# Performance work log

Measured on AMD Instinct MI355X. Metric: run time of the kernel, lower is better.

The kernel has to match this reference:

```python
import jax, jax.numpy as jnp
import numpy as np
import math

D_MODEL = 2048
N_HEADS = 16
HEAD_DIM = D_MODEL // N_HEADS  # 128
SEQ = 2048
BATCH = 1


def make_freqs(seq_len, head_dim, theta=10000.0):
    # standard rotary frequencies: freqs_cis = exp(i * t * inv_freq)
    inv_freq = 1.0 / (theta ** (np.arange(0, head_dim, 2, dtype=np.float32) / head_dim))
    t = np.arange(seq_len, dtype=np.float32)
    ang = np.outer(t, inv_freq)  # [seq, head_dim/2]
    return jnp.asarray(np.cos(ang)), jnp.asarray(np.sin(ang))


def setup_inputs() -> dict:
    key = jax.random.key(0)
    ks = jax.random.split(key, 6)
    x = jax.random.normal(ks[0], (BATCH, SEQ, D_MODEL), dtype=jnp.float32)
    freqs_cos, freqs_sin = make_freqs(SEQ, HEAD_DIM)
    # causal additive mask, broadcastable to [b, h, s, s]
    mask = jnp.where(jnp.tril(jnp.ones((SEQ, SEQ), dtype=bool)), 0.0, -1e9).astype(jnp.float32)[None, None]
    scale = 0.02
    wq = jax.random.normal(ks[1], (D_MODEL, D_MODEL), dtype=jnp.float32) * scale
    wk = jax.random.normal(ks[2], (D_MODEL, D_MODEL), dtype=jnp.float32) * scale
    wv = jax.random.normal(ks[3], (D_MODEL, D_MODEL), dtype=jnp.float32) * scale
    wo = jax.random.normal(ks[4], (D_MODEL, D_MODEL), dtype=jnp.float32) * scale
    return {"x": x, "freqs_cos": freqs_cos, "freqs_sin": freqs_sin, "mask": mask,
            "wq": wq, "wk": wk, "wv": wv, "wo": wo}


def _apply_rotary(q, k, cos, sin):
    # q, k: [b, s, h, hd]; cos/sin: [s, hd/2]
    def rot(t):
        tr = t.reshape(*t.shape[:-1], -1, 2)  # [b, s, h, hd/2, 2]
        re, im = tr[..., 0], tr[..., 1]
        c = cos[None, :, None, :]
        s = sin[None, :, None, :]
        # complex multiply (re + i im) * (c + i s)
        out_re = re * c - im * s
        out_im = re * s + im * c
        return jnp.stack([out_re, out_im], axis=-1).reshape(t.shape)
    return rot(q), rot(k)


def reference(x, freqs_cos, freqs_sin, mask, wq, wk, wv, wo):
    b, s, _ = x.shape
    # QKV projections (nn.Linear with no bias: x @ W^T; W is square so use x @ W
    # with W stored already-transposed -- weights here are random so x @ W is faithful math)
    q = (x @ wq).reshape(b, s, N_HEADS, HEAD_DIM)
    k = (x @ wk).reshape(b, s, N_HEADS, HEAD_DIM)
    v = (x @ wv).reshape(b, s, N_HEADS, HEAD_DIM)
    q, k = _apply_rotary(q, k, freqs_cos, freqs_sin)
    # [b, h, s_q, s_k]
    scores = jnp.einsum("bqhd,bkhd->bhqk", q, k) / math.sqrt(HEAD_DIM)
    scores = scores + mask
    probs = jax.nn.softmax(scores.astype(jnp.float32), axis=-1).astype(q.dtype)
    out = jnp.einsum("bhqk,bkhd->bqhd", probs, v).reshape(b, s, N_HEADS * HEAD_DIM)
    return out @ wo
```

## Files before the change

### kernel.cpp

```cpp
#include <hip/hip_runtime.h>
#include <hip/hip_bf16.h>
#include <math.h>

#define SEQ 2048
#define DM 2048
#define NH 16
#define HD 128
#define QKV_N 6144

typedef __bf16 bf16;
typedef __bf16 bf16x8 __attribute__((ext_vector_type(8)));
typedef __bf16 bf16x4v __attribute__((ext_vector_type(4)));
typedef __bf16 bf16x2v __attribute__((ext_vector_type(2)));
typedef float f32x4 __attribute__((ext_vector_type(4)));

__device__ inline int sw_idx(int row, int quad) {
    return (row * 4 + (quad ^ ((row >> 1) & 3))) * 8;
}

__device__ inline void async16(const void* g, void* l) {
    __builtin_amdgcn_global_load_lds((const __attribute__((address_space(1))) void*)g,
                                     (__attribute__((address_space(3))) void*)l, 16, 0, 0);
}

__global__ void k_convert_x(const float* __restrict__ x, bf16* __restrict__ xb) {
    int i = blockIdx.x * 256 + threadIdx.x;
    float4 v = ((const float4*)x)[i];
    bf16x4v o;
    o.x = (bf16)v.x; o.y = (bf16)v.y; o.z = (bf16)v.z; o.w = (bf16)v.w;
    ((bf16x4v*)xb)[i] = o;
}

__global__ void k_transpose_w4(const float* __restrict__ wq, const float* __restrict__ wk,
                               const float* __restrict__ wv, const float* __restrict__ wo,
                               bf16* __restrict__ wT, bf16* __restrict__ woT) {
    __shared__ float tile[32][33];
    const int z = blockIdx.z;
    const float* src = (z == 0) ? wq : (z == 1) ? wk : (z == 2) ? wv : wo;
    bf16* dst = (z < 3) ? (wT + (size_t)z * DM * DM) : woT;
    int tx = threadIdx.x, ty = threadIdx.y;
    int bx = blockIdx.x * 32, by = blockIdx.y * 32;
    tile[ty][tx] = src[(size_t)(by + ty) * DM + bx + tx];
    __syncthreads();
    dst[(size_t)(bx + ty) * DM + by + tx] = (bf16)tile[tx][ty];
}

__global__ void k_post(bf16* __restrict__ qkv, const float* __restrict__ cosT,
                       const float* __restrict__ sinT, bf16* __restrict__ vT) {
    __shared__ bf16 tile[32][33];
    int tx = threadIdx.x, ty = threadIdx.y;
    if (blockIdx.y < 64) {
        int bx = blockIdx.x * 32, by = blockIdx.y * 32;
        tile[ty][tx] = qkv[(size_t)(by + ty) * QKV_N + 2 * DM + bx + tx];
        __syncthreads();
        vT[(size_t)(bx + ty) * SEQ + by + tx] = tile[tx][ty];
    } else {
        int b = (blockIdx.y - 64) * 64 + blockIdx.x;
        int idx = b * 1024 + ty * 32 + tx;
        int i = idx & 63;
        int h = (idx >> 6) & 15;
        int s = idx >> 10;
        float c = cosT[s * 64 + i], sn = sinT[s * 64 + i];
        size_t base = (size_t)s * QKV_N + h * HD + 2 * i;
        bf16x2v q = *(bf16x2v*)&qkv[base];
        float qr = (float)q.x, qi = (float)q.y;
        bf16x2v qo;
        qo.x = (bf16)(qr * c - qi * sn);
        qo.y = (bf16)(qr * sn + qi * c);
        *(bf16x2v*)&qkv[base] = qo;
        bf16x2v k = *(bf16x2v*)&qkv[base + DM];
        float kr = (float)k.x, ki = (float)k.y;
        bf16x2v ko;
        ko.x = (bf16)(kr * c - ki * sn);
        ko.y = (bf16)(kr * sn + ki * c);
        *(bf16x2v*)&qkv[base + DM] = ko;
    }
}

template <typename OutT, int BN>
__global__ __launch_bounds__(256) void k_gemm_bt(const bf16* __restrict__ A,
                                                 const bf16* __restrict__ Bt,
                                                 OutT* __restrict__ C,
                                                 int M, int N, int K) {
    constexpr int NI = BN / 32;
    __shared__ bf16 As[128 * 32];
    __shared__ bf16 Bs[BN * 32];
    const int t = threadIdx.x;
    const int lane = t & 63;
    const int w = t >> 6;
    const int wr = (w >> 1) * 64, wc = (w & 1) * (BN / 2);
    const int l15 = lane & 15, quad = lane >> 4;
    const size_t bm = (size_t)blockIdx.y * 128, bn = (size_t)blockIdx.x * BN;
    f32x4 acc[4][NI];
#pragma unroll
    for (int i = 0; i < 4; ++i)
#pragma unroll
        for (int j = 0; j < NI; ++j) acc[i][j] = (f32x4){0.f, 0.f, 0.f, 0.f};

    const int row0 = t >> 2, row1 = 64 + (t >> 2);
    const int ch = ((t & 3) ^ ((t >> 3) & 3)) * 8;

    for (int kt = 0; kt < K; kt += 32) {
        async16(&A[(bm + row0) * K + kt + ch], &As[t * 8]);
        async16(&A[(bm + row1) * K + kt + ch], &As[(t + 256) * 8]);
        async16(&Bt[(bn + row0) * K + kt + ch], &Bs[t * 8]);
        if (BN == 128)
            async16(&Bt[(bn + row1) * K + kt + ch], &Bs[(t + 256) * 8]);
        __syncthreads();
        bf16x8 af[4], bfm[NI];
#pragma unroll
        for (int mi = 0; mi < 4; ++mi)
            af[mi] = *(const bf16x8*)&As[sw_idx(wr + mi * 16 + l15, quad)];
#pragma unroll
        for (int ni = 0; ni < NI; ++ni)
            bfm[ni] = *(const bf16x8*)&Bs[sw_idx(wc + ni * 16 + l15, quad)];
#pragma unroll
        for (int mi = 0; mi < 4; ++mi)
#pragma unroll
            for (int ni = 0; ni < NI; ++ni)
                acc[mi][ni] = __builtin_amdgcn_mfma_f32_16x16x32_bf16(
                    af[mi], bfm[ni], acc[mi][ni], 0, 0, 0);
        __syncthreads();
    }
#pragma unroll
    for (int mi = 0; mi < 4; ++mi)
#pragma unroll
        for (int ni = 0; ni < NI; ++ni)
#pragma unroll
            for (int r = 0; r < 4; ++r) {
                size_t row = bm + wr + mi * 16 + quad * 4 + r;
                size_t col = bn + wc + ni * 16 + l15;
                C[row * (size_t)N + col] = (OutT)acc[mi][ni][r];
            }
}

__global__ __launch_bounds__(256) void k_flash(const bf16* __restrict__ qkv,
                                               const bf16* __restrict__ vT,
                                               bf16* __restrict__ out) {
    __shared__ bf16 Ks[4][64 * 32];
    __shared__ bf16 Vs[2][128 * 32];
    __shared__ bf16 Pl[4][16][72];
    const int t = threadIdx.x;
    const int lane = t & 63;
    const int w = t >> 6;
    const int l15 = lane & 15, quad = lane >> 4;
    const int b = blockIdx.x;
    const int h = (b & 7) * 2 + ((b >> 3) & 1);
    const int qb = 31 - (b >> 4);
    const int q0w = qb * 64 + w * 16;
    const float sc = 0.08838834764831845f;

    const size_t qrow = (size_t)(q0w + l15) * QKV_N + h * HD;
    bf16x8 aq[4];
#pragma unroll
    for (int u = 0; u < 4; ++u)
        aq[u] = *(const bf16x8*)&qkv[qrow + u * 32 + quad * 8];

    f32x4 o[8];
#pragma unroll
    for (int c = 0; c < 8; ++c) o[c] = (f32x4){0.f, 0.f, 0.f, 0.f};
    float l_r[4] = {0.f, 0.f, 0.f, 0.f};

    const int srow = t >> 2;
    const int ch = ((t & 3) ^ ((t >> 3) & 3)) * 8;

    for (int kt = 0; kt <= qb; ++kt) {
        const int kbase = kt * 64;
#pragma unroll
        for (int u = 0; u < 4; ++u)
            async16(&qkv[(size_t)(kbase + srow) * QKV_N + DM + h * HD + u * 32 + ch],
                    &Ks[u][t * 8]);
#pragma unroll
        for (int j = 0; j < 2; ++j) {
            async16(&vT[(size_t)(h * HD + srow) * SEQ + kbase + j * 32 + ch],
                    &Vs[j][t * 8]);
            async16(&vT[(size_t)(h * HD + 64 + srow) * SEQ + kbase + j * 32 + ch],
                    &Vs[j][(t + 256) * 8]);
        }
        __syncthreads();
        f32x4 s[4];
#pragma unroll
        for (int sub = 0; sub < 4; ++sub) {
            f32x4 z = (f32x4){0.f, 0.f, 0.f, 0.f};
#pragma unroll
            for (int u = 0; u < 4; ++u) {
                bf16x8 kb = *(const bf16x8*)&Ks[u][sw_idx(sub * 16 + l15, quad)];
                z = __builtin_amdgcn_mfma_f32_16x16x32_bf16(aq[u], kb, z, 0, 0, 0);
            }
            s[sub] = z;
        }
        const bool masked = (kt == qb);
#pragma unroll
        for (int sub = 0; sub < 4; ++sub)
#pragma unroll
            for (int r = 0; r < 4; ++r) {
                float p = __expf(s[sub][r] * sc);
                if (masked)
                    p = (kbase + sub * 16 + l15 <= q0w + quad * 4 + r) ? p : 0.f;
                l_r[r] += p;
                Pl[w][quad * 4 + r][sub * 16 + l15] = (bf16)p;
            }
        __syncthreads();
        bf16x8 pf0 = *(const bf16x8*)&Pl[w][l15][quad * 8];
        bf16x8 pf1 = *(const bf16x8*)&Pl[w][l15][32 + quad * 8];
#pragma unroll
        for (int c = 0; c < 8; ++c) {
            bf16x8 vb0 = *(const bf16x8*)&Vs[0][sw_idx(c * 16 + l15, quad)];
            o[c] = __builtin_amdgcn_mfma_f32_16x16x32_bf16(pf0, vb0, o[c], 0, 0, 0);
            bf16x8 vb1 = *(const bf16x8*)&Vs[1][sw_idx(c * 16 + l15, quad)];
            o[c] = __builtin_amdgcn_mfma_f32_16x16x32_bf16(pf1, vb1, o[c], 0, 0, 0);
        }
        __syncthreads();
    }

    float rl[4];
#pragma unroll
    for (int r = 0; r < 4; ++r) {
        float l = l_r[r];
        l += __shfl_xor(l, 1, 16);
        l += __shfl_xor(l, 2, 16);
        l += __shfl_xor(l, 4, 16);
        l += __shfl_xor(l, 8, 16);
        rl[r] = 1.0f / l;
    }
#pragma unroll
    for (int c = 0; c < 8; ++c)
#pragma unroll
        for (int r = 0; r < 4; ++r)
            out[(size_t)(q0w + quad * 4 + r) * DM + h * HD + c * 16 + l15] =
                (bf16)(o[c][r] * rl[r]);
}

extern "C" void kernel_launch(void* const* d_in, const int* in_sizes, int n_in,
                              void* d_out, int out_size, void* d_ws, size_t ws_size,
                              hipStream_t stream) {
    const float* x  = (const float*)d_in[0];
    const float* fc = (const float*)d_in[1];
    const float* fs = (const float*)d_in[2];
    const float* wq = (const float*)d_in[4];
    const float* wk = (const float*)d_in[5];
    const float* wv = (const float*)d_in[6];
    const float* wo = (const float*)d_in[7];
    float* out = (float*)d_out;

    char* ws = (char*)d_ws;
    bf16* xb  = (bf16*)(ws);
    bf16* wT  = (bf16*)(ws + (size_t)(8u  << 20));
    bf16* woT = (bf16*)(ws + (size_t)(32u << 20));
    bf16* qkv = (bf16*)(ws + (size_t)(40u << 20));
    bf16* vT  = (bf16*)(ws + (size_t)(64u << 20));

    k_convert_x<<<4096, 256, 0, stream>>>(x, xb);
    k_transpose_w4<<<dim3(64, 64, 4), dim3(32, 32), 0, stream>>>(wq, wk, wv, wo, wT, woT);
    k_gemm_bt<bf16, 128><<<dim3(48, 16), 256, 0, stream>>>(xb, wT, qkv, SEQ, QKV_N, DM);
    k_post<<<dim3(64, 96), dim3(32, 32), 0, stream>>>(qkv, fc, fs, vT);
    k_flash<<<512, 256, 0, stream>>>(qkv, vT, xb);
    k_gemm_bt<float, 64><<<dim3(32, 16), 256, 0, stream>>>(xb, woT, out, SEQ, DM, DM);
}
```

Baseline: 331.0 us.

## Deepen GEMM K-tile to 64, split-K output projection, merge prep kernels

The GEMM kernel now loads 64-wide K tiles with an 8-chunk XOR swizzle, which halves the number of barriers per K step. The output projection uses 128x128 tiles with a 2-way split-K, accumulated by float atomics into an output that is zeroed by a memset first. The x conversion is folded into the weight transpose launch to remove one kernel launch. In exchange, the GEMM uses more LDS per block and the split-K adds atomic traffic plus a memset.

Result: no change. 331.1 us (+0.0%).

```diff
diff --git a/kernel.cpp b/kernel.cpp
--- a/kernel.cpp
+++ b/kernel.cpp
@@ -14,8 +14,11 @@
 typedef __bf16 bf16x2v __attribute__((ext_vector_type(2)));
 typedef float f32x4 __attribute__((ext_vector_type(4)));
 
-__device__ inline int sw_idx(int row, int quad) {
+__device__ inline int sw_idx32(int row, int quad) {
     return (row * 4 + (quad ^ ((row >> 1) & 3))) * 8;
+}
+__device__ inline int sw_idx64(int row, int chunk) {
+    return (row * 8 + (chunk ^ (row & 7))) * 8;
 }
 
 __device__ inline void async16(const void* g, void* l) {
@@ -23,22 +26,25 @@
                                      (__attribute__((address_space(3))) void*)l, 16, 0, 0);
 }
 
-__global__ void k_convert_x(const float* __restrict__ x, bf16* __restrict__ xb) {
-    int i = blockIdx.x * 256 + threadIdx.x;
-    float4 v = ((const float4*)x)[i];
-    bf16x4v o;
-    o.x = (bf16)v.x; o.y = (bf16)v.y; o.z = (bf16)v.z; o.w = (bf16)v.w;
-    ((bf16x4v*)xb)[i] = o;
-}
-
-__global__ void k_transpose_w4(const float* __restrict__ wq, const float* __restrict__ wk,
-                               const float* __restrict__ wv, const float* __restrict__ wo,
-                               bf16* __restrict__ wT, bf16* __restrict__ woT) {
+__global__ void k_prep(const float* __restrict__ wq, const float* __restrict__ wk,
+                       const float* __restrict__ wv, const float* __restrict__ wo,
+                       bf16* __restrict__ wT, bf16* __restrict__ woT,
+                       const float* __restrict__ x, bf16* __restrict__ xb) {
+    const int z = blockIdx.z;
+    int tx = threadIdx.x, ty = threadIdx.y;
+    if (z == 4) {
+        int bid = blockIdx.y * 64 + blockIdx.x;
+        if (bid >= 1024) return;
+        int i = bid * 1024 + ty * 32 + tx;
+        float4 v = ((const float4*)x)[i];
+        bf16x4v o;
+        o.x = (bf16)v.x; o.y = (bf16)v.y; o.z = (bf16)v.z; o.w = (bf16)v.w;
+        ((bf16x4v*)xb)[i] = o;
+        return;
+    }
     __shared__ float tile[32][33];
-    const int z = blockIdx.z;
     const float* src = (z == 0) ? wq : (z == 1) ? wk : (z == 2) ? wv : wo;
     bf16* dst = (z < 3) ? (wT + (size_t)z * DM * DM) : woT;
-    int tx = threadIdx.x, ty = threadIdx.y;
     int bx = blockIdx.x * 32, by = blockIdx.y * 32;
     tile[ty][tx] = src[(size_t)(by + ty) * DM + bx + tx];
     __syncthreads();
@@ -77,60 +83,73 @@
     }
 }
 
-template <typename OutT, int BN>
+template <typename OutT, int KSPLIT>
 __global__ __launch_bounds__(256) void k_gemm_bt(const bf16* __restrict__ A,
                                                  const bf16* __restrict__ Bt,
                                                  OutT* __restrict__ C,
                                                  int M, int N, int K) {
-    constexpr int NI = BN / 32;
-    __shared__ bf16 As[128 * 32];
-    __shared__ bf16 Bs[BN * 32];
+    __shared__ bf16 As[128 * 64];
+    __shared__ bf16 Bs[128 * 64];
     const int t = threadIdx.x;
     const int lane = t & 63;
     const int w = t >> 6;
-    const int wr = (w >> 1) * 64, wc = (w & 1) * (BN / 2);
+    const int wr = (w >> 1) * 64, wc = (w & 1) * 64;
     const int l15 = lane & 15, quad = lane >> 4;
-    const size_t bm = (size_t)blockIdx.y * 128, bn = (size_t)blockIdx.x * BN;
-    f32x4 acc[4][NI];
+    const size_t bm = (size_t)blockIdx.y * 128, bn = (size_t)blockIdx.x * 128;
+    const int Kb = K / KSPLIT;
+    const int k0 = (KSPLIT > 1) ? (int)blockIdx.z * Kb : 0;
+    f32x4 acc[4][4];
 #pragma unroll
     for (int i = 0; i < 4; ++i)
 #pragma unroll
-        for (int j = 0; j < NI; ++j) acc[i][j] = (f32x4){0.f, 0.f, 0.f, 0.f};
-
-    const int row0 = t >> 2, row1 = 64 + (t >> 2);
-    const int ch = ((t & 3) ^ ((t >> 3) & 3)) * 8;
-
-    for (int kt = 0; kt < K; kt += 32) {
-        async16(&A[(bm + row0) * K + kt + ch], &As[t * 8]);
-        async16(&A[(bm + row1) * K + kt + ch], &As[(t + 256) * 8]);
-        async16(&Bt[(bn + row0) * K + kt + ch], &Bs[t * 8]);
-        if (BN == 128)
-            async16(&Bt[(bn + row1) * K + kt + ch], &Bs[(t + 256) * 8]);
-        __syncthreads();
-        bf16x8 af[4], bfm[NI];
-#pragma unroll
-        for (int mi = 0; mi < 4; ++mi)
-            af[mi] = *(const bf16x8*)&As[sw_idx(wr + mi * 16 + l15, quad)];
-#pragma unroll
-        for (int ni = 0; ni < NI; ++ni)
-            bfm[ni] = *(const bf16x8*)&Bs[sw_idx(wc + ni * 16 + l15, quad)];
-#pragma unroll
-        for (int mi = 0; mi < 4; ++mi)
-#pragma unroll
-            for (int ni = 0; ni < NI; ++ni)
-                acc[mi][ni] = __builtin_amdgcn_mfma_f32_16x16x32_bf16(
-                    af[mi], bfm[ni], acc[mi][ni], 0, 0, 0);
+        for (int j = 0; j < 4; ++j) acc[i][j] = (f32x4){0.f, 0.f, 0.f, 0.f};
+
+    int srow[4], sgc[4];
+#pragma unroll
+    for (int j = 0; j < 4; ++j) {
+        int c = j * 256 + t;
+        srow[j] = c >> 3;
+        sgc[j] = ((c & 7) ^ (srow[j] & 7)) * 8;
+    }
+
+    for (int kt = 0; kt < Kb; kt += 64) {
+#pragma unroll
+        for (int j = 0; j < 4; ++j) {
+            async16(&A[(bm + srow[j]) * K + k0 + kt + sgc[j]], &As[(j * 256 + t) * 8]);
+            async16(&Bt[(bn + srow[j]) * K + k0 + kt + sgc[j]], &Bs[(j * 256 + t) * 8]);
+        }
+        __syncthreads();
+#pragma unroll
+        for (int kh = 0; kh < 2; ++kh) {
+            bf16x8 af[4], bfm[4];
+#pragma unroll
+            for (int mi = 0; mi < 4; ++mi)
+                af[mi] = *(const bf16x8*)&As[sw_idx64(wr + mi * 16 + l15, kh * 4 + quad)];
+#pragma unroll
+            for (int ni = 0; ni < 4; ++ni)
+                bfm[ni] = *(const bf16x8*)&Bs[sw_idx64(wc + ni * 16 + l15, kh * 4 + quad)];
+#pragma unroll
+            for (int mi = 0; mi < 4; ++mi)
+#pragma unroll
+                for (int ni = 0; ni < 4; ++ni)
+                    acc[mi][ni] = __builtin_amdgcn_mfma_f32_16x16x32_bf16(
+                        af[mi], bfm[ni], acc[mi][ni], 0, 0, 0);
+        }
         __syncthreads();
     }
 #pragma unroll
     for (int mi = 0; mi < 4; ++mi)
 #pragma unroll
-        for (int ni = 0; ni < NI; ++ni)
+        for (int ni = 0; ni < 4; ++ni)
 #pragma unroll
             for (int r = 0; r < 4; ++r) {
                 size_t row = bm + wr + mi * 16 + quad * 4 + r;
                 size_t col = bn + wc + ni * 16 + l15;
-                C[row * (size_t)N + col] = (OutT)acc[mi][ni][r];
+                if (KSPLIT > 1)
+                    unsafeAtomicAdd((float*)&C[row * (size_t)N + col],
+                                    (float)acc[mi][ni][r]);
+                else
+                    C[row * (size_t)N + col] = (OutT)acc[mi][ni][r];
             }
 }
 
@@ -184,7 +203,7 @@
             f32x4 z = (f32x4){0.f, 0.f, 0.f, 0.f};
 #pragma unroll
             for (int u = 0; u < 4; ++u) {
-                bf16x8 kb = *(const bf16x8*)&Ks[u][sw_idx(sub * 16 + l15, quad)];
+                bf16x8 kb = *(const bf16x8*)&Ks[u][sw_idx32(sub * 16 + l15, quad)];
                 z = __builtin_amdgcn_mfma_f32_16x16x32_bf16(aq[u], kb, z, 0, 0, 0);
             }
             s[sub] = z;
@@ -205,9 +224,9 @@
         bf16x8 pf1 = *(const bf16x8*)&Pl[w][l15][32 + quad * 8];
 #pragma unroll
         for (int c = 0; c < 8; ++c) {
-            bf16x8 vb0 = *(const bf16x8*)&Vs[0][sw_idx(c * 16 + l15, quad)];
+            bf16x8 vb0 = *(const bf16x8*)&Vs[0][sw_idx32(c * 16 + l15, quad)];
             o[c] = __builtin_amdgcn_mfma_f32_16x16x32_bf16(pf0, vb0, o[c], 0, 0, 0);
-            bf16x8 vb1 = *(const bf16x8*)&Vs[1][sw_idx(c * 16 + l15, quad)];
+            bf16x8 vb1 = *(const bf16x8*)&Vs[1][sw_idx32(c * 16 + l15, quad)];
             o[c] = __builtin_amdgcn_mfma_f32_16x16x32_bf16(pf1, vb1, o[c], 0, 0, 0);
         }
         __syncthreads();
@@ -250,10 +269,10 @@
     bf16* qkv = (bf16*)(ws + (size_t)(40u << 20));
     bf16* vT  = (bf16*)(ws + (size_t)(64u << 20));
 
-    k_convert_x<<<4096, 256, 0, stream>>>(x, xb);
-    k_transpose_w4<<<dim3(64, 64, 4), dim3(32, 32), 0, stream>>>(wq, wk, wv, wo, wT, woT);
-    k_gemm_bt<bf16, 128><<<dim3(48, 16), 256, 0, stream>>>(xb, wT, qkv, SEQ, QKV_N, DM);
+    hipMemsetAsync(out, 0, (size_t)SEQ * DM * sizeof(float), stream);
+    k_prep<<<dim3(64, 64, 5), dim3(32, 32), 0, stream>>>(wq, wk, wv, wo, wT, woT, x, xb);
+    k_gemm_bt<bf16, 1><<<dim3(48, 16), 256, 0, stream>>>(xb, wT, qkv, SEQ, QKV_N, DM);
     k_post<<<dim3(64, 96), dim3(32, 32), 0, stream>>>(qkv, fc, fs, vT);
     k_flash<<<512, 256, 0, stream>>>(qkv, vT, xb);
-    k_gemm_bt<float, 64><<<dim3(32, 16), 256, 0, stream>>>(xb, woT, out, SEQ, DM, DM);
-}
+    k_gemm_bt<float, 2><<<dim3(16, 16, 2), 256, 0, stream>>>(xb, woT, out, SEQ, DM, DM);
+}
```
